# Kernel optimization log

Measured on AMD Instinct MI355X. Metric: run time of the kernel, lower is better.

## Reference

```python
import jax, jax.numpy as jnp
import numpy as np

B, H, S, D = 4, 8, 2048, 64

def setup_inputs() -> dict:
    key = jax.random.key(0)
    k1, k2 = jax.random.split(key)
    q = jax.random.normal(k1, (B, H, S, D), dtype=jnp.float32)
    kv = jax.random.normal(k2, (B, H, S, D), dtype=jnp.float32)
    mask = jnp.zeros((1, 1, S, S), dtype=jnp.float32)
    return {"q": q, "kv": kv, "mask": mask}

def reference(q, kv, mask):
    # score = q @ kv^T / sqrt(d_k) + mask ; softmax over last dim ; @ kv
    d_k = jnp.asarray(kv.shape[-1], dtype=q.dtype)
    score = jnp.einsum('bhqd,bhkd->bhqk', q, kv) / jnp.sqrt(d_k)
    score = score + mask
    attn = jax.nn.softmax(score, axis=-1)
    out = jnp.einsum('bhqk,bhkd->bhqd', attn, kv)
    return out
```

## Files before the change

### kernel.cpp

```cpp
#include <hip/hip_runtime.h>
#include <hip/hip_bf16.h>
#include <stdint.h>


typedef __bf16 bf16;
typedef __attribute__((ext_vector_type(8))) __bf16 bf16x8;
typedef __attribute__((ext_vector_type(4))) __bf16 bf16x4;
typedef __attribute__((ext_vector_type(4))) float floatx4;
typedef __attribute__((ext_vector_type(16))) float floatx16;
typedef __attribute__((ext_vector_type(4))) int int4v;
typedef __attribute__((ext_vector_type(2))) unsigned int uint2v;

#define SLEN 2048
#define DH   64
#define BR   64
#define BC   64
#define NKT  (SLEN / BC)
#define NEP  (NKT / 2)
#define NQT  (SLEN / BR)
#define BH_N 32
#define LOG2E 1.44269504088896341f

#define CHB_L  1024
#define IMGB_L 8192
#define IMGE_G 4096
#define BUF2   (4 * IMGB_L)

#define AS1 __attribute__((address_space(1)))
#define AS3 __attribute__((address_space(3)))

static __device__ inline void gload_lds16(const void* g, void* l) {
    __builtin_amdgcn_global_load_lds((const AS1 uint32_t*)g, (AS3 uint32_t*)l, 16, 0, 0);
}

static __device__ inline float fexp2(float x) {
    return __builtin_amdgcn_exp2f(x);
}

static_assert(BH_N == NQT, "prep kernel folds bh and qt onto one grid axis");

__global__ __launch_bounds__(256) void kv_prep(
    const float* __restrict__ kv, const float* __restrict__ mask,
    bf16* __restrict__ kvK, bf16* __restrict__ kvT, int* __restrict__ flags)
{
    __shared__ bf16 Tl[64 * 72];
    __shared__ int wany[4];
    const int kt = blockIdx.x, z = blockIdx.y;
    const int t = threadIdx.x;

    float acc = 0.f;
#pragma unroll
    for (int i = 0; i < 4; ++i) {
        int f = i * 256 + t;
        int row = f >> 4, c4 = (f & 15) * 4;
        const float4 v = *(const float4*)(mask + (size_t)(z * BR + row) * SLEN + kt * BC + c4);
        acc = fmaxf(acc, fmaxf(fmaxf(fabsf(v.x), fabsf(v.y)), fmaxf(fabsf(v.z), fabsf(v.w))));
    }
    unsigned long long any = __ballot(acc != 0.f);
    if ((t & 63) == 0) wany[t >> 6] = (any != 0ull) ? 1 : 0;

    const float* src = kv + ((size_t)z * SLEN + kt * BC) * DH;
#pragma unroll
    for (int i = 0; i < 4; ++i) {
        int f = i * 256 + t;
        int key = f >> 4, d4 = (f & 15) * 4;
        float4 v = *(const float4*)(src + (size_t)key * DH + d4);
        bf16x4 b; b[0] = (bf16)v.x; b[1] = (bf16)v.y; b[2] = (bf16)v.z; b[3] = (bf16)v.w;
        *(bf16x4*)&Tl[key * 72 + d4] = b;
    }
    __syncthreads();
    if (t == 0) flags[z * NKT + kt] = wany[0] | wany[1] | wany[2] | wany[3];

    bf16* outK = kvK + ((size_t)z * NKT + kt) * IMGE_G;
#pragma unroll
    for (int i = 0; i < 2; ++i) {
        int G = i * 256 + t;
        int c = G >> 6, L = G & 63, rl = L >> 3, p = L & 7;
        int g = (p - rl - 4 * (c & 1)) & 7, key = 8 * c + rl;
        bf16x8 w = *(const bf16x8*)&Tl[key * 72 + g * 8];
        *(bf16x8*)(outK + (size_t)G * 8) = w;
    }
    bf16* outV = kvT + ((size_t)z * NKT + kt) * IMGE_G;
#pragma unroll
    for (int i = 0; i < 2; ++i) {
        int G = i * 256 + t;
        int c = G >> 6, L = G & 63, dl = L >> 3, p = L & 7;
        int g = (p - dl - 4 * (c & 1)) & 7, d = 8 * c + dl;
        bf16x8 w;
#pragma unroll
        for (int j = 0; j < 8; ++j)
            w[j] = Tl[(8 * g + j) * 72 + d];
        *(bf16x8*)(outV + (size_t)G * 8) = w;
    }
}

__global__ __launch_bounds__(256, 2) void attn_fwd14(
    const float* __restrict__ q, const float* __restrict__ mask,
    const int* __restrict__ flags,
    const bf16* __restrict__ kvK, const bf16* __restrict__ kvT,
    float* __restrict__ out)
{
    __shared__ __align__(16) char smem[2 * BUF2];

    const int bh = blockIdx.x;
    const int qt = blockIdx.y;
    const int q0 = qt * 128;
    const int t = threadIdx.x;
    const int w = t >> 6, lane = t & 63;
    const int r5 = lane & 31, h = lane >> 5;
    const int c3 = r5 >> 3, rl = lane & 7;

    const float qscale = 0.125f * LOG2E;
    bf16x8 qf[4];
    {
        const float* qrow = q + ((size_t)bh * SLEN + q0 + w * 32 + r5) * DH;
#pragma unroll
        for (int s = 0; s < 4; ++s) {
            float4 f0 = *(const float4*)(qrow + 16 * s + 8 * h);
            float4 f1 = *(const float4*)(qrow + 16 * s + 8 * h + 4);
            bf16x8 a;
            a[0] = (bf16)(f0.x * qscale); a[1] = (bf16)(f0.y * qscale);
            a[2] = (bf16)(f0.z * qscale); a[3] = (bf16)(f0.w * qscale);
            a[4] = (bf16)(f1.x * qscale); a[5] = (bf16)(f1.y * qscale);
            a[6] = (bf16)(f1.z * qscale); a[7] = (bf16)(f1.w * qscale);
            qf[s] = a;
        }
    }

    const int fqt = qt * 2 + (w >> 1);
    unsigned fmask;
    {
        int ld = (lane < 32) ? flags[fqt * NKT + lane] : 0;
        fmask = (unsigned)__ballot(ld != 0);
    }

    int addr4[4];
#pragma unroll
    for (int s = 0; s < 4; ++s) {
        int slot = (2 * s + h + rl + 4 * (c3 & 1)) & 7;
        addr4[s] = c3 * 1024 + rl * 128 + slot * 16;
    }

    floatx16 o[2];
#pragma unroll
    for (int dt = 0; dt < 2; ++dt)
#pragma unroll
        for (int i = 0; i < 16; ++i) o[dt][i] = 0.f;
    float m_run = -3.0e38f, l_run = 0.f;

    const bf16* kvKb = kvK + (size_t)bh * NKT * IMGE_G;
    const bf16* kvTb = kvT + (size_t)bh * NKT * IMGE_G;

    auto stage = [&](int t2, char* Bn) {
        const bf16* gK = kvKb + (size_t)t2 * IMGE_G;
        const bf16* gV = kvTb + (size_t)t2 * IMGE_G;
#pragma unroll
        for (int cc = 0; cc < 2; ++cc) {
            const int c = 2 * w + cc;
            gload_lds16(gK + (size_t)c * 512 + lane * 8,          Bn +              c * CHB_L);
            gload_lds16(gV + (size_t)c * 512 + lane * 8,          Bn + IMGB_L +     c * CHB_L);
            gload_lds16(gK + IMGE_G + (size_t)c * 512 + lane * 8, Bn + 2 * IMGB_L + c * CHB_L);
            gload_lds16(gV + IMGE_G + (size_t)c * 512 + lane * 8, Bn + 3 * IMGB_L + c * CHB_L);
        }
    };

    stage(0, smem);

    for (int e = 0; e < NEP; ++e) {
        __syncthreads();

        if (e + 1 < NEP) stage(2 * e + 2, smem + ((e + 1) & 1) * BUF2);

        const char* B = smem + (e & 1) * BUF2;

        floatx16 s[4];
#pragma unroll
        for (int T = 0; T < 4; ++T) {
            const char* Kimg = B + (T >> 1) * (2 * IMGB_L) + (T & 1) * 4096;
            floatx16 acc;
#pragma unroll
            for (int i = 0; i < 16; ++i) acc[i] = 0.f;
#pragma unroll
            for (int ss = 0; ss < 4; ++ss) {
                bf16x8 kf = *(const bf16x8*)(Kimg + addr4[ss]);
                acc = __builtin_amdgcn_mfma_f32_32x32x16_bf16(kf, qf[ss], acc, 0, 0, 0);
            }
            s[T] = acc;
        }

#pragma unroll
        for (int T = 0; T < 4; ++T) {
            if (fmask & (1u << (2 * e + (T >> 1)))) {
                const float* mrow = mask + (size_t)(q0 + w * 32 + r5) * SLEN
                                    + e * 128 + T * 32 + 4 * h;
#pragma unroll
                for (int g4 = 0; g4 < 4; ++g4) {
                    float4 mv = *(const float4*)(mrow + 8 * g4);
                    s[T][4 * g4 + 0] += mv.x * LOG2E;
                    s[T][4 * g4 + 1] += mv.y * LOG2E;
                    s[T][4 * g4 + 2] += mv.z * LOG2E;
                    s[T][4 * g4 + 3] += mv.w * LOG2E;
                }
            }
        }

        float tm[4];
#pragma unroll
        for (int T = 0; T < 4; ++T) {
            float a0 = fmaxf(s[T][0], s[T][1]),   a1 = fmaxf(s[T][2], s[T][3]);
            float a2 = fmaxf(s[T][4], s[T][5]),   a3 = fmaxf(s[T][6], s[T][7]);
            float a4 = fmaxf(s[T][8], s[T][9]),   a5 = fmaxf(s[T][10], s[T][11]);
            float a6 = fmaxf(s[T][12], s[T][13]), a7 = fmaxf(s[T][14], s[T][15]);
            a0 = fmaxf(a0, a1); a2 = fmaxf(a2, a3); a4 = fmaxf(a4, a5); a6 = fmaxf(a6, a7);
            tm[T] = fmaxf(fmaxf(a0, a2), fmaxf(a4, a6));
        }
        float tmax = fmaxf(fmaxf(tm[0], tm[1]), fmaxf(tm[2], tm[3]));
        tmax = fmaxf(tmax, __shfl_xor(tmax, 32));
        float mnew = fmaxf(m_run, tmax);
        unsigned long long grew = __ballot(mnew > m_run);
        float alpha = fexp2(m_run - mnew);
        m_run = mnew;
        if (grew) {
#pragma unroll
            for (int dt = 0; dt < 2; ++dt)
#pragma unroll
                for (int i = 0; i < 16; ++i) o[dt][i] *= alpha;
        }

        float rs = 0.f;
#pragma unroll
        for (int T = 0; T < 4; ++T) {
            float ev[16];
#pragma unroll
            for (int i = 0; i < 16; ++i) ev[i] = fexp2(s[T][i] - mnew);
            float r0 = (ev[0] + ev[1]) + (ev[2] + ev[3]);
            float r1 = (ev[4] + ev[5]) + (ev[6] + ev[7]);
            float r2 = (ev[8] + ev[9]) + (ev[10] + ev[11]);
            float r3 = (ev[12] + ev[13]) + (ev[14] + ev[15]);
            rs += (r0 + r1) + (r2 + r3);

            bf16x4 lA = { (bf16)ev[0],  (bf16)ev[1],  (bf16)ev[2],  (bf16)ev[3]  };
            bf16x4 hA = { (bf16)ev[4],  (bf16)ev[5],  (bf16)ev[6],  (bf16)ev[7]  };
            bf16x4 lB = { (bf16)ev[8],  (bf16)ev[9],  (bf16)ev[10], (bf16)ev[11] };
            bf16x4 hB = { (bf16)ev[12], (bf16)ev[13], (bf16)ev[14], (bf16)ev[15] };
            uint2v xA = __builtin_bit_cast(uint2v, lA);
            uint2v yA = __builtin_bit_cast(uint2v, hA);
            uint2v xB = __builtin_bit_cast(uint2v, lB);
            uint2v yB = __builtin_bit_cast(uint2v, hB);
            uint2v sA0 = __builtin_amdgcn_permlane32_swap(xA[0], yA[0], false, false);
            uint2v sA1 = __builtin_amdgcn_permlane32_swap(xA[1], yA[1], false, false);
            uint2v sB0 = __builtin_amdgcn_permlane32_swap(xB[0], yB[0], false, false);
            uint2v sB1 = __builtin_amdgcn_permlane32_swap(xB[1], yB[1], false, false);
            int4v pAi = { (int)sA0[0], (int)sA1[0], (int)sA0[1], (int)sA1[1] };
            int4v pBi = { (int)sB0[0], (int)sB1[0], (int)sB0[1], (int)sB1[1] };
            bf16x8 pfA = __builtin_bit_cast(bf16x8, pAi);
            bf16x8 pfB = __builtin_bit_cast(bf16x8, pBi);

            const char* Vimg = B + IMGB_L + (T >> 1) * (2 * IMGB_L);
            const int uA = 2 * (T & 1), uB = uA + 1;
#pragma unroll
            for (int dt = 0; dt < 2; ++dt) {
                bf16x8 vA = *(const bf16x8*)(Vimg + dt * 4096 + addr4[uA]);
                o[dt] = __builtin_amdgcn_mfma_f32_32x32x16_bf16(vA, pfA, o[dt], 0, 0, 0);
                bf16x8 vB = *(const bf16x8*)(Vimg + dt * 4096 + addr4[uB]);
                o[dt] = __builtin_amdgcn_mfma_f32_32x32x16_bf16(vB, pfB, o[dt], 0, 0, 0);
            }
        }
        rs += __shfl_xor(rs, 32);
        l_run = (grew ? l_run * alpha : l_run) + rs;
    }

    const float inv = 1.0f / l_run;
    float* ob = out + ((size_t)bh * SLEN + q0 + w * 32 + r5) * DH + 4 * h;
#pragma unroll
    for (int dt = 0; dt < 2; ++dt)
#pragma unroll
        for (int k = 0; k < 4; ++k) {
            float4 v;
            v.x = o[dt][4 * k + 0] * inv;
            v.y = o[dt][4 * k + 1] * inv;
            v.z = o[dt][4 * k + 2] * inv;
            v.w = o[dt][4 * k + 3] * inv;
            *(float4*)(ob + dt * 32 + 8 * k) = v;
        }
}

#define LDT 72
__global__ __launch_bounds__(256) void attn_mask_flags(
    const float* __restrict__ mask, int* __restrict__ flags)
{
    const int kt = blockIdx.x, qt = blockIdx.y;
    const int t = threadIdx.x;
    float acc = 0.f;
#pragma unroll
    for (int i = 0; i < 4; ++i) {
        int f = i * 256 + t;
        int row = f >> 4, c4 = (f & 15) * 4;
        const float4 v = *(const float4*)(mask + (size_t)(qt * BR + row) * SLEN + kt * BC + c4);
        acc = fmaxf(acc, fmaxf(fmaxf(fabsf(v.x), fabsf(v.y)), fmaxf(fabsf(v.z), fabsf(v.w))));
    }
    unsigned long long any = __ballot(acc != 0.f);
    __shared__ int wany[4];
    if ((t & 63) == 0) wany[t >> 6] = (any != 0ull) ? 1 : 0;
    __syncthreads();
    if (t == 0) flags[qt * NKT + kt] = wany[0] | wany[1] | wany[2] | wany[3];
}

__global__ __launch_bounds__(256) void attn_fwd(
    const float* __restrict__ q, const float* __restrict__ kv,
    const float* __restrict__ mask, const int* __restrict__ flags,
    float* __restrict__ out)
{
    __shared__ __align__(16) bf16 Kl[BC * LDT];
    __shared__ __align__(16) bf16 Vt[DH * LDT];
    __shared__ __align__(16) bf16 Pl[BR * LDT];

    const int qt = blockIdx.x;
    const int bh = blockIdx.y;
    const int q0 = qt * BR;
    const int t = threadIdx.x;
    const int wave = t >> 6, lane = t & 63;
    const int ln16 = lane & 15, quad = lane >> 4;

    const float qscale = 0.125f * LOG2E;
    bf16x8 aq[2];
    {
        const float* qrow = q + ((size_t)bh * SLEN + q0 + wave * 16 + ln16) * DH;
#pragma unroll
        for (int kc = 0; kc < 2; ++kc) {
            float4 f0 = *(const float4*)(qrow + kc * 32 + quad * 8);
            float4 f1 = *(const float4*)(qrow + kc * 32 + quad * 8 + 4);
            bf16x8 a;
            a[0] = (bf16)(f0.x * qscale); a[1] = (bf16)(f0.y * qscale);
            a[2] = (bf16)(f0.z * qscale); a[3] = (bf16)(f0.w * qscale);
            a[4] = (bf16)(f1.x * qscale); a[5] = (bf16)(f1.y * qscale);
            a[6] = (bf16)(f1.z * qscale); a[7] = (bf16)(f1.w * qscale);
            aq[kc] = a;
        }
    }

    floatx4 o[4];
#pragma unroll
    for (int dt = 0; dt < 4; ++dt) o[dt] = (floatx4){0.f, 0.f, 0.f, 0.f};
    float m_run[4], l_run[4];
#pragma unroll
    for (int r = 0; r < 4; ++r) { m_run[r] = -3.0e38f; l_run[r] = 0.f; }

    const float* kvb = kv + (size_t)bh * SLEN * DH;

    for (int kt = 0; kt < NKT; ++kt) {
        float4 st[4];
        const float* kvt = kvb + (size_t)kt * BC * DH;
#pragma unroll
        for (int i = 0; i < 4; ++i) {
            int f = i * 256 + t;
            st[i] = *(const float4*)(kvt + (size_t)f * 4);
        }
        __syncthreads();
#pragma unroll
        for (int i = 0; i < 4; ++i) {
            int f = i * 256 + t;
            int key = f >> 4, d4 = (f & 15) * 4;
            bf16 b0 = (bf16)st[i].x, b1 = (bf16)st[i].y, b2 = (bf16)st[i].z, b3 = (bf16)st[i].w;
            *(bf16x4*)&Kl[key * LDT + d4] = (bf16x4){b0, b1, b2, b3};
            Vt[(d4 + 0) * LDT + key] = b0;
            Vt[(d4 + 1) * LDT + key] = b1;
            Vt[(d4 + 2) * LDT + key] = b2;
            Vt[(d4 + 3) * LDT + key] = b3;
        }
        __syncthreads();

        floatx4 s[4];
#pragma unroll
        for (int nt = 0; nt < 4; ++nt) {
            s[nt] = (floatx4){0.f, 0.f, 0.f, 0.f};
#pragma unroll
            for (int kc = 0; kc < 2; ++kc) {
                bf16x8 bk = *(const bf16x8*)&Kl[(ln16 + 16 * nt) * LDT + kc * 32 + quad * 8];
                s[nt] = __builtin_amdgcn_mfma_f32_16x16x32_bf16(aq[kc], bk, s[nt], 0, 0, 0);
            }
        }

        if (!flags || flags[qt * NKT + kt]) {
            const float* mrow = mask + (size_t)(q0 + quad * 4) * SLEN + kt * BC + ln16;
#pragma unroll
            for (int r = 0; r < 4; ++r)
#pragma unroll
                for (int nt = 0; nt < 4; ++nt)
                    s[nt][r] += mrow[(size_t)r * SLEN + nt * 16] * LOG2E;
        }

#pragma unroll
        for (int r = 0; r < 4; ++r) {
            float mx = fmaxf(fmaxf(s[0][r], s[1][r]), fmaxf(s[2][r], s[3][r]));
            mx = fmaxf(mx, __shfl_xor(mx, 1));
            mx = fmaxf(mx, __shfl_xor(mx, 2));
            mx = fmaxf(mx, __shfl_xor(mx, 4));
            mx = fmaxf(mx, __shfl_xor(mx, 8));
            float mnew = fmaxf(m_run[r], mx);
            float alpha = exp2f(m_run[r] - mnew);
            m_run[r] = mnew;
            float rs = 0.f;
#pragma unroll
            for (int nt = 0; nt < 4; ++nt) {
                float p = exp2f(s[nt][r] - mnew);
                s[nt][r] = p;
                rs += p;
            }
            rs += __shfl_xor(rs, 1);
            rs += __shfl_xor(rs, 2);
            rs += __shfl_xor(rs, 4);
            rs += __shfl_xor(rs, 8);
            l_run[r] = l_run[r] * alpha + rs;
#pragma unroll
            for (int dt = 0; dt < 4; ++dt) o[dt][r] *= alpha;
        }

#pragma unroll
        for (int nt = 0; nt < 4; ++nt)
#pragma unroll
            for (int r = 0; r < 4; ++r)
                Pl[(wave * 16 + quad * 4 + r) * LDT + ln16 + 16 * nt] = (bf16)s[nt][r];

#pragma unroll
        for (int kc2 = 0; kc2 < 2; ++kc2) {
            bf16x8 pfr = *(const bf16x8*)&Pl[(wave * 16 + ln16) * LDT + kc2 * 32 + quad * 8];
#pragma unroll
            for (int dt = 0; dt < 4; ++dt) {
                bf16x8 vfr = *(const bf16x8*)&Vt[(ln16 + 16 * dt) * LDT + kc2 * 32 + quad * 8];
                o[dt] = __builtin_amdgcn_mfma_f32_16x16x32_bf16(pfr, vfr, o[dt], 0, 0, 0);
            }
        }
    }

#pragma unroll
    for (int r = 0; r < 4; ++r) {
        float inv = 1.0f / l_run[r];
        int qrow = q0 + wave * 16 + quad * 4 + r;
        float* orow = out + ((size_t)bh * SLEN + qrow) * DH;
#pragma unroll
        for (int dt = 0; dt < 4; ++dt)
            orow[ln16 + 16 * dt] = o[dt][r] * inv;
    }
}

extern "C" void kernel_launch(void* const* d_in, const int* in_sizes, int n_in,
                              void* d_out, int out_size, void* d_ws, size_t ws_size,
                              hipStream_t stream)
{
    const float* q    = (const float*)d_in[0];
    const float* kv   = (const float*)d_in[1];
    const float* mask = (const float*)d_in[2];
    float* out = (float*)d_out;

    const size_t kvKoff = 4096;
    const size_t kvToff = kvKoff + (size_t)BH_N * NKT * IMGE_G * 2;
    const size_t need   = kvToff + (size_t)BH_N * NKT * IMGE_G * 2;

    if (ws_size >= need) {
        int*  flags = (int*)d_ws;
        bf16* kvK   = (bf16*)((char*)d_ws + kvKoff);
        bf16* kvT   = (bf16*)((char*)d_ws + kvToff);
        kv_prep<<<dim3(NKT, BH_N), 256, 0, stream>>>(kv, mask, kvK, kvT, flags);
        attn_fwd14<<<dim3(BH_N, SLEN / 128), 256, 0, stream>>>(q, mask, flags, kvK, kvT, out);
    } else {
        int* flags = nullptr;
        if (ws_size >= (size_t)NQT * NKT * sizeof(int)) {
            flags = (int*)d_ws;
            attn_mask_flags<<<dim3(NKT, NQT), 256, 0, stream>>>(mask, flags);
        }
        attn_fwd<<<dim3(NQT, BH_N), 256, 0, stream>>>(q, kv, mask, flags, out);
    }
}
```

Before: 141.6 us.

## Split key tiles across two wave groups per block and merge softmax states

```diff
diff --git a/kernel.cpp b/kernel.cpp
--- a/kernel.cpp
+++ b/kernel.cpp
@@ -94,7 +94,7 @@
     }
 }
 
-__global__ __launch_bounds__(256, 2) void attn_fwd14(
+__global__ __launch_bounds__(512, 4) void attn_fwd15(
     const float* __restrict__ q, const float* __restrict__ mask,
     const int* __restrict__ flags,
     const bf16* __restrict__ kvK, const bf16* __restrict__ kvT,
@@ -107,13 +107,14 @@
     const int q0 = qt * 128;
     const int t = threadIdx.x;
     const int w = t >> 6, lane = t & 63;
+    const int qg = w & 3, kh = w >> 2;
     const int r5 = lane & 31, h = lane >> 5;
     const int c3 = r5 >> 3, rl = lane & 7;
 
     const float qscale = 0.125f * LOG2E;
     bf16x8 qf[4];
     {
-        const float* qrow = q + ((size_t)bh * SLEN + q0 + w * 32 + r5) * DH;
+        const float* qrow = q + ((size_t)bh * SLEN + q0 + qg * 32 + r5) * DH;
 #pragma unroll
         for (int s = 0; s < 4; ++s) {
             float4 f0 = *(const float4*)(qrow + 16 * s + 8 * h);
@@ -127,7 +128,7 @@
         }
     }
 
-    const int fqt = qt * 2 + (w >> 1);
+    const int fqt = qt * 2 + (qg >> 1);
     unsigned fmask;
     {
         int ld = (lane < 32) ? flags[fqt * NKT + lane] : 0;
@@ -154,14 +155,10 @@
     auto stage = [&](int t2, char* Bn) {
         const bf16* gK = kvKb + (size_t)t2 * IMGE_G;
         const bf16* gV = kvTb + (size_t)t2 * IMGE_G;
-#pragma unroll
-        for (int cc = 0; cc < 2; ++cc) {
-            const int c = 2 * w + cc;
-            gload_lds16(gK + (size_t)c * 512 + lane * 8,          Bn +              c * CHB_L);
-            gload_lds16(gV + (size_t)c * 512 + lane * 8,          Bn + IMGB_L +     c * CHB_L);
-            gload_lds16(gK + IMGE_G + (size_t)c * 512 + lane * 8, Bn + 2 * IMGB_L + c * CHB_L);
-            gload_lds16(gV + IMGE_G + (size_t)c * 512 + lane * 8, Bn + 3 * IMGB_L + c * CHB_L);
-        }
+        gload_lds16(gK + (size_t)w * 512 + lane * 8,          Bn +              w * CHB_L);
+        gload_lds16(gV + (size_t)w * 512 + lane * 8,          Bn + IMGB_L +     w * CHB_L);
+        gload_lds16(gK + IMGE_G + (size_t)w * 512 + lane * 8, Bn + 2 * IMGB_L + w * CHB_L);
+        gload_lds16(gV + IMGE_G + (size_t)w * 512 + lane * 8, Bn + 3 * IMGB_L + w * CHB_L);
     };
 
     stage(0, smem);
@@ -173,29 +170,31 @@
 
         const char* B = smem + (e & 1) * BUF2;
 
-        floatx16 s[4];
-#pragma unroll
-        for (int T = 0; T < 4; ++T) {
-            const char* Kimg = B + (T >> 1) * (2 * IMGB_L) + (T & 1) * 4096;
+        floatx16 s[2];
+#pragma unroll
+        for (int T = 0; T < 2; ++T) {
+            const char* Kimg = B + kh * (2 * IMGB_L) + T * 4096;
             floatx16 acc;
 #pragma unroll
             for (int i = 0; i < 16; ++i) acc[i] = 0.f;
+            __builtin_amdgcn_s_setprio(1);
 #pragma unroll
             for (int ss = 0; ss < 4; ++ss) {
                 bf16x8 kf = *(const bf16x8*)(Kimg + addr4[ss]);
                 acc = __builtin_amdgcn_mfma_f32_32x32x16_bf16(kf, qf[ss], acc, 0, 0, 0);
             }
+            __builtin_amdgcn_s_setprio(0);
             s[T] = acc;
         }
 
-#pragma unroll
-        for (int T = 0; T < 4; ++T) {
-            if (fmask & (1u << (2 * e + (T >> 1)))) {
-                const float* mrow = mask + (size_t)(q0 + w * 32 + r5) * SLEN
-                                    + e * 128 + T * 32 + 4 * h;
+        if (fmask & (1u << (2 * e + kh))) {
+            const float* mbase = mask + (size_t)(q0 + qg * 32 + r5) * SLEN
+                                 + (2 * e + kh) * 64 + 4 * h;
+#pragma unroll
+            for (int T = 0; T < 2; ++T) {
 #pragma unroll
                 for (int g4 = 0; g4 < 4; ++g4) {
-                    float4 mv = *(const float4*)(mrow + 8 * g4);
+                    float4 mv = *(const float4*)(mbase + T * 32 + 8 * g4);
                     s[T][4 * g4 + 0] += mv.x * LOG2E;
                     s[T][4 * g4 + 1] += mv.y * LOG2E;
                     s[T][4 * g4 + 2] += mv.z * LOG2E;
@@ -204,9 +203,9 @@
             }
         }
 
-        float tm[4];
-#pragma unroll
-        for (int T = 0; T < 4; ++T) {
+        float tm[2];
+#pragma unroll
+        for (int T = 0; T < 2; ++T) {
             float a0 = fmaxf(s[T][0], s[T][1]),   a1 = fmaxf(s[T][2], s[T][3]);
             float a2 = fmaxf(s[T][4], s[T][5]),   a3 = fmaxf(s[T][6], s[T][7]);
             float a4 = fmaxf(s[T][8], s[T][9]),   a5 = fmaxf(s[T][10], s[T][11]);
@@ -214,7 +213,7 @@
             a0 = fmaxf(a0, a1); a2 = fmaxf(a2, a3); a4 = fmaxf(a4, a5); a6 = fmaxf(a6, a7);
             tm[T] = fmaxf(fmaxf(a0, a2), fmaxf(a4, a6));
         }
-        float tmax = fmaxf(fmaxf(tm[0], tm[1]), fmaxf(tm[2], tm[3]));
+        float tmax = fmaxf(tm[0], tm[1]);
         tmax = fmaxf(tmax, __shfl_xor(tmax, 32));
         float mnew = fmaxf(m_run, tmax);
         unsigned long long grew = __ballot(mnew > m_run);
@@ -228,8 +227,9 @@
         }
 
         float rs = 0.f;
-#pragma unroll
-        for (int T = 0; T < 4; ++T) {
+        const char* Vimg = B + IMGB_L + kh * (2 * IMGB_L);
+#pragma unroll
+        for (int T = 0; T < 2; ++T) {
             float ev[16];
 #pragma unroll
             for (int i = 0; i < 16; ++i) ev[i] = fexp2(s[T][i] - mnew);
@@ -256,8 +256,8 @@
             bf16x8 pfA = __builtin_bit_cast(bf16x8, pAi);
             bf16x8 pfB = __builtin_bit_cast(bf16x8, pBi);
 
-            const char* Vimg = B + IMGB_L + (T >> 1) * (2 * IMGB_L);
-            const int uA = 2 * (T & 1), uB = uA + 1;
+            const int uA = 2 * T, uB = 2 * T + 1;
+            __builtin_amdgcn_s_setprio(1);
 #pragma unroll
             for (int dt = 0; dt < 2; ++dt) {
                 bf16x8 vA = *(const bf16x8*)(Vimg + dt * 4096 + addr4[uA]);
@@ -265,24 +265,49 @@
                 bf16x8 vB = *(const bf16x8*)(Vimg + dt * 4096 + addr4[uB]);
                 o[dt] = __builtin_amdgcn_mfma_f32_32x32x16_bf16(vB, pfB, o[dt], 0, 0, 0);
             }
+            __builtin_amdgcn_s_setprio(0);
         }
         rs += __shfl_xor(rs, 32);
         l_run = (grew ? l_run * alpha : l_run) + rs;
     }
 
-    const float inv = 1.0f / l_run;
-    float* ob = out + ((size_t)bh * SLEN + q0 + w * 32 + r5) * DH + 4 * h;
-#pragma unroll
-    for (int dt = 0; dt < 2; ++dt)
-#pragma unroll
-        for (int k = 0; k < 4; ++k) {
-            float4 v;
-            v.x = o[dt][4 * k + 0] * inv;
-            v.y = o[dt][4 * k + 1] * inv;
-            v.z = o[dt][4 * k + 2] * inv;
-            v.w = o[dt][4 * k + 3] * inv;
-            *(float4*)(ob + dt * 32 + 8 * k) = v;
-        }
+    __syncthreads();
+    float* Obuf = (float*)smem;
+    float* MLb  = (float*)(smem + 32768);
+    if (kh == 1) {
+#pragma unroll
+        for (int dt = 0; dt < 2; ++dt)
+#pragma unroll
+            for (int k = 0; k < 4; ++k) {
+                float4 v;
+                v.x = o[dt][4 * k + 0]; v.y = o[dt][4 * k + 1];
+                v.z = o[dt][4 * k + 2]; v.w = o[dt][4 * k + 3];
+                *(float4*)(Obuf + ((size_t)(qg * 8 + dt * 4 + k) * 64 + lane) * 4) = v;
+            }
+        float2 ml; ml.x = m_run; ml.y = l_run;
+        *(float2*)(MLb + ((size_t)qg * 64 + lane) * 2) = ml;
+    }
+    __syncthreads();
+    if (kh == 0) {
+        float2 ml = *(const float2*)(MLb + ((size_t)qg * 64 + lane) * 2);
+        float m = fmaxf(m_run, ml.x);
+        float a0 = fexp2(m_run - m), a1 = fexp2(ml.x - m);
+        float l = l_run * a0 + ml.y * a1;
+        float inv = 1.f / l;
+        float* ob = out + ((size_t)bh * SLEN + q0 + qg * 32 + r5) * DH + 4 * h;
+#pragma unroll
+        for (int dt = 0; dt < 2; ++dt)
+#pragma unroll
+            for (int k = 0; k < 4; ++k) {
+                float4 p = *(const float4*)(Obuf + ((size_t)(qg * 8 + dt * 4 + k) * 64 + lane) * 4);
+                float4 v;
+                v.x = (o[dt][4 * k + 0] * a0 + p.x * a1) * inv;
+                v.y = (o[dt][4 * k + 1] * a0 + p.y * a1) * inv;
+                v.z = (o[dt][4 * k + 2] * a0 + p.z * a1) * inv;
+                v.w = (o[dt][4 * k + 3] * a0 + p.w * a1) * inv;
+                *(float4*)(ob + dt * 32 + 8 * k) = v;
+            }
+    }
 }
 
 #define LDT 72
@@ -462,7 +487,7 @@
         bf16* kvK   = (bf16*)((char*)d_ws + kvKoff);
         bf16* kvT   = (bf16*)((char*)d_ws + kvToff);
         kv_prep<<<dim3(NKT, BH_N), 256, 0, stream>>>(kv, mask, kvK, kvT, flags);
-        attn_fwd14<<<dim3(BH_N, SLEN / 128), 256, 0, stream>>>(q, mask, flags, kvK, kvT, out);
+        attn_fwd15<<<dim3(BH_N, SLEN / 128), 512, 0, stream>>>(q, mask, flags, kvK, kvT, out);
     } else {
         int* flags = nullptr;
         if (ws_size >= (size_t)NQT * NKT * sizeof(int)) {
```

Result: slower. 145.7 us (+2.9%).
